# Performance work log

Hardware: AMD Instinct MI355X
Metric: run time of the kernel (lower is better)

The kernel has to match this reference:

```python
import jax, jax.numpy as jnp
import numpy as np

N = 50000      # nodes
E = 800000     # edges (avg degree 16)
IN_DIM = 128
HID = 64       # num_hidden
HEADS = 1
NUM_LAYERS = 3       # -> 4 SNATConv layers total
SLOPE = 0.2          # negative_slope
THR = 0.01           # threhold: edges with attention < THR are pruned after layer 0


def setup_inputs() -> dict:
    key = jax.random.key(0)
    ks = jax.random.split(key, 16)
    s = 0.05
    x = jax.random.normal(ks[0], (N, IN_DIM), jnp.float32)
    edge_src = jax.random.randint(ks[1], (E,), 0, N)
    edge_dst = jax.random.randint(ks[2], (E,), 0, N)
    W_embed = jax.random.normal(ks[3], (IN_DIM, HID), jnp.float32) * s
    n_conv = NUM_LAYERS + 1
    # all conv layers map HID*HEADS -> HEADS*HID (heads==1 so square)
    W_gat = jax.random.normal(ks[4], (n_conv, HID, HEADS * HID), jnp.float32) * s
    a_l = jax.random.normal(ks[5], (n_conv, HEADS, HID), jnp.float32) * s
    a_r = jax.random.normal(ks[6], (n_conv, HEADS, HID), jnp.float32) * s
    d_cat = (NUM_LAYERS + 1) * HID
    W0 = jax.random.normal(ks[7], (d_cat, HID), jnp.float32) * s
    b0 = jnp.zeros((HID,), jnp.float32)
    W1 = jax.random.normal(ks[8], (HID, HID), jnp.float32) * s
    b1 = jnp.zeros((HID,), jnp.float32)
    W2 = jax.random.normal(ks[9], (HID, 1), jnp.float32) * s
    b2 = jnp.zeros((1,), jnp.float32)
    return {"x": x, "edge_src": edge_src, "edge_dst": edge_dst,
            "W_embed": W_embed, "W_gat": W_gat, "a_l": a_l, "a_r": a_r,
            "W0": W0, "b0": b0, "W1": W1, "b1": b1, "W2": W2, "b2": b2}


def _edge_softmax(e, dst):
    # e: [E, H] raw scores; softmax over incoming edges of each dst node
    m = jax.ops.segment_max(e, dst, num_segments=N)       # [N, H]
    a = jnp.exp(e - m[dst])
    s = jax.ops.segment_sum(a, dst, num_segments=N)       # [N, H]
    return a / jnp.maximum(s[dst], 1e-9)


def _snat_conv(h, W, al, ar, src, dst, mask):
    # h: [N, F_in]; W: [F_in, H*HID]; al/ar: [H, HID]
    feat = (h @ W).reshape(N, HEADS, HID)                 # [N, H, HID]
    el = jnp.sum(feat * al, axis=-1)                      # [N, H]
    er = jnp.sum(feat * ar, axis=-1)
    e = jax.nn.leaky_relu(el[src] + er[dst], SLOPE)       # [E, H]
    if mask is not None:
        e = jnp.where(mask, e, -1e9)                      # prune thresholded edges
    alpha = _edge_softmax(e, dst)                         # [E, H]
    out = jax.ops.segment_sum(feat[src] * alpha[..., None], dst, num_segments=N)
    return jax.nn.elu(out), alpha                         # [N, H, HID], [E, H]


def reference(x, edge_src, edge_dst, W_embed, W_gat, a_l, a_r, W0, b0, W1, b1, W2, b2):
    src, dst = edge_src, edge_dst
    h = jnp.tanh(x @ W_embed)                             # [N, HID]
    # layer 0: computes attention and the threshold mask (index_1 / index_0)
    h0, alpha = _snat_conv(h, W_gat[0], a_l[0], a_r[0], src, dst, None)
    mask = alpha >= THR                                   # [E, H] kept-edge mask
    h = h0.reshape(N, HEADS * HID)
    H_cat = [h]
    for l in range(1, NUM_LAYERS):                        # middle layers reuse mask
        hl, _ = _snat_conv(h, W_gat[l], a_l[l], a_r[l], src, dst, mask)
        h = hl.reshape(N, HEADS * HID)
        H_cat.append(h)
    feats, _ = _snat_conv(h, W_gat[NUM_LAYERS], a_l[NUM_LAYERS], a_r[NUM_LAYERS], src, dst, mask)
    feats = feats.mean(axis=1)                            # [N, HID] mean over heads
    f = jnp.concatenate(H_cat + [feats], axis=1)          # [N, (L+1)*HID]
    out = jax.nn.relu(f @ W0 + b0)                        # activationP
    out = jax.nn.relu(out @ W1 + b1)
    out = jax.nn.relu(out @ W2 + b2)                      # final F.relu
    return out                                            # [N, 1]
```

## Files before the change

kernel.cpp:

```cpp
#include <hip/hip_runtime.h>
#include <math.h>


__global__ void k_zero(int* __restrict__ counts, int N) {
  int i = blockIdx.x * 256 + threadIdx.x;
  if (i < N) counts[i] = 0;
}

__global__ void k_hist(const int* __restrict__ dst, int* __restrict__ counts, int E) {
  int e = blockIdx.x * blockDim.x + threadIdx.x;
  if (e < E) atomicAdd(&counts[dst[e]], 1);
}

__global__ __launch_bounds__(1024) void k_bsum(const int* __restrict__ counts,
                                               int* __restrict__ bsum, int n) {
  __shared__ int wsum[16];
  int tid = threadIdx.x, lane = tid & 63, wid = tid >> 6;
  int i = blockIdx.x * 1024 + tid;
  int v = (i < n) ? counts[i] : 0;
  #pragma unroll
  for (int off = 32; off; off >>= 1) v += __shfl_xor(v, off, 64);
  if (lane == 0) wsum[wid] = v;
  __syncthreads();
  if (wid == 0) {
    int w = (lane < 16) ? wsum[lane] : 0;
    #pragma unroll
    for (int off = 8; off; off >>= 1) w += __shfl_xor(w, off, 64);
    if (lane == 0) bsum[blockIdx.x] = w;
  }
}

__global__ __launch_bounds__(64) void k_bscan(const int* __restrict__ bsum,
                                              int* __restrict__ bofs,
                                              int* __restrict__ row_ptr,
                                              int nb, int n) {
  int lane = threadIdx.x;
  int carry = 0;
  for (int base = 0; base < nb; base += 64) {
    int idx = base + lane;
    int orig = (idx < nb) ? bsum[idx] : 0;
    int inc = orig;
    #pragma unroll
    for (int off = 1; off < 64; off <<= 1) {
      int t = __shfl_up(inc, off, 64);
      if (lane >= off) inc += t;
    }
    if (idx < nb) bofs[idx] = carry + inc - orig;
    carry += __shfl(inc, 63, 64);
  }
  if (lane == 0) row_ptr[n] = carry;
}

__global__ __launch_bounds__(1024) void k_scan3(const int* __restrict__ counts,
                                                const int* __restrict__ bofs,
                                                int* __restrict__ row_ptr,
                                                int* __restrict__ cursor, int n) {
  __shared__ int wsum[16];
  int tid = threadIdx.x, lane = tid & 63, wid = tid >> 6;
  int i = blockIdx.x * 1024 + tid;
  int v = (i < n) ? counts[i] : 0;
  int inc = v;
  #pragma unroll
  for (int off = 1; off < 64; off <<= 1) {
    int t = __shfl_up(inc, off, 64);
    if (lane >= off) inc += t;
  }
  if (lane == 63) wsum[wid] = inc;
  __syncthreads();
  if (wid == 0 && lane < 16) {
    int orig = wsum[lane];
    int w = orig;
    #pragma unroll
    for (int off = 1; off < 16; off <<= 1) {
      int t = __shfl_up(w, off, 64);
      if (lane >= off) w += t;
    }
    wsum[lane] = w - orig;
  }
  __syncthreads();
  int excl = bofs[blockIdx.x] + wsum[wid] + inc - v;
  if (i < n) { row_ptr[i] = excl; cursor[i] = excl; }
}

__global__ void k_scatter(const int* __restrict__ src, const int* __restrict__ dst,
                          int* __restrict__ cursor, int* __restrict__ csr_src, int E) {
  int e = blockIdx.x * blockDim.x + threadIdx.x;
  if (e < E) {
    int pos = atomicAdd(&cursor[dst[e]], 1);
    csr_src[pos] = src[e];
  }
}

#define SWS 68

#define STAGE_W(DST, SRC)                                            \
  {                                                                  \
    int k_ = threadIdx.x >> 2, p_ = threadIdx.x & 3;                 \
    const float* s_ = (SRC) + k_ * 64 + p_ * 16;                     \
    float* d_ = (DST) + k_ * SWS + p_ * 16;                          \
    _Pragma("unroll")                                                \
    for (int c_ = 0; c_ < 4; c_++)                                   \
      *(float4*)(d_ + c_ * 4) = *(const float4*)(s_ + c_ * 4);       \
  }

#define GEMM64(ACC, ABASE, ASTRIDE, KOFF)                            \
  { _Pragma("unroll 4")                                              \
    for (int k_ = 0; k_ < 64; k_++) {                                \
      float4 w4_ = *(const float4*)&sW[k_ * SWS + fq];               \
      float a0_ = (ABASE)[(nr +  0) * (ASTRIDE) + (KOFF) + k_];      \
      float a1_ = (ABASE)[(nr + 16) * (ASTRIDE) + (KOFF) + k_];      \
      float a2_ = (ABASE)[(nr + 32) * (ASTRIDE) + (KOFF) + k_];      \
      float a3_ = (ABASE)[(nr + 48) * (ASTRIDE) + (KOFF) + k_];      \
      ACC[0][0] = fmaf(a0_, w4_.x, ACC[0][0]);                       \
      ACC[0][1] = fmaf(a0_, w4_.y, ACC[0][1]);                       \
      ACC[0][2] = fmaf(a0_, w4_.z, ACC[0][2]);                       \
      ACC[0][3] = fmaf(a0_, w4_.w, ACC[0][3]);                       \
      ACC[1][0] = fmaf(a1_, w4_.x, ACC[1][0]);                       \
      ACC[1][1] = fmaf(a1_, w4_.y, ACC[1][1]);                       \
      ACC[1][2] = fmaf(a1_, w4_.z, ACC[1][2]);                       \
      ACC[1][3] = fmaf(a1_, w4_.w, ACC[1][3]);                       \
      ACC[2][0] = fmaf(a2_, w4_.x, ACC[2][0]);                       \
      ACC[2][1] = fmaf(a2_, w4_.y, ACC[2][1]);                       \
      ACC[2][2] = fmaf(a2_, w4_.z, ACC[2][2]);                       \
      ACC[2][3] = fmaf(a2_, w4_.w, ACC[2][3]);                       \
      ACC[3][0] = fmaf(a3_, w4_.x, ACC[3][0]);                       \
      ACC[3][1] = fmaf(a3_, w4_.y, ACC[3][1]);                       \
      ACC[3][2] = fmaf(a3_, w4_.z, ACC[3][2]);                       \
      ACC[3][3] = fmaf(a3_, w4_.w, ACC[3][3]);                       \
    } }

__global__ __launch_bounds__(256, 3) void k_embed_feat(
    const float* __restrict__ x, const float* __restrict__ We,
    const float* __restrict__ Wg, const float* __restrict__ al,
    const float* __restrict__ ar, float* __restrict__ feat,
    float* __restrict__ el, float* __restrict__ er, int N) {
  __shared__ float sA[64 * 129];
  __shared__ float sW[64 * SWS];
  __shared__ float sE[64 * 8];
  int tid = threadIdx.x, lane = tid & 63, wv = tid >> 6;
  int nb0 = blockIdx.x * 64, nl = N - 1;
  int r = tid >> 2, p = tid & 3;
  int nr = lane >> 2, fc = lane & 3;
  int fq = wv * 16 + fc * 4;
  {
    const float* gp = x + (size_t)min(nb0 + r, nl) * 128;
    #pragma unroll
    for (int half = 0; half < 2; half++) {
      const float* g = gp + half * 64 + p * 16;
      float4 v0 = *(const float4*)(g + 0), v1 = *(const float4*)(g + 4);
      float4 v2 = *(const float4*)(g + 8), v3 = *(const float4*)(g + 12);
      float* dp = &sA[r * 129 + half * 64 + p * 16];
      dp[0]=v0.x; dp[1]=v0.y; dp[2]=v0.z; dp[3]=v0.w;
      dp[4]=v1.x; dp[5]=v1.y; dp[6]=v1.z; dp[7]=v1.w;
      dp[8]=v2.x; dp[9]=v2.y; dp[10]=v2.z; dp[11]=v2.w;
      dp[12]=v3.x; dp[13]=v3.y; dp[14]=v3.z; dp[15]=v3.w;
    }
  }
  STAGE_W(sW, We);
  __syncthreads();
  float acc[4][4];
  #pragma unroll
  for (int m = 0; m < 4; m++)
    #pragma unroll
    for (int j = 0; j < 4; j++) acc[m][j] = 0.f;
  GEMM64(acc, sA, 129, 0);
  __syncthreads();
  STAGE_W(sW, We + 4096);
  __syncthreads();
  GEMM64(acc, sA, 129, 64);
  __syncthreads();
  STAGE_W(sW, Wg);
  #pragma unroll
  for (int m = 0; m < 4; m++)
    #pragma unroll
    for (int j = 0; j < 4; j++)
      sA[(nr + 16 * m) * 65 + fq + j] = tanhf(acc[m][j]);
  __syncthreads();
  float acc2[4][4];
  #pragma unroll
  for (int m = 0; m < 4; m++)
    #pragma unroll
    for (int j = 0; j < 4; j++) acc2[m][j] = 0.f;
  GEMM64(acc2, sA, 65, 0);
  {
    float alv[4], arv[4];
    *(float4*)&alv[0] = *(const float4*)(al + fq);
    *(float4*)&arv[0] = *(const float4*)(ar + fq);
    #pragma unroll
    for (int m = 0; m < 4; m++) {
      float pl = 0.f, pr = 0.f;
      #pragma unroll
      for (int j = 0; j < 4; j++) {
        pl = fmaf(acc2[m][j], alv[j], pl);
        pr = fmaf(acc2[m][j], arv[j], pr);
      }
      pl += __shfl_xor(pl, 1, 64); pl += __shfl_xor(pl, 2, 64);
      pr += __shfl_xor(pr, 1, 64); pr += __shfl_xor(pr, 2, 64);
      if (fc == 0) {
        sE[(nr + 16 * m) * 8 + wv] = pl;
        sE[(nr + 16 * m) * 8 + 4 + wv] = pr;
      }
    }
  }
  __syncthreads();
  #pragma unroll
  for (int m = 0; m < 4; m++)
    #pragma unroll
    for (int j = 0; j < 4; j++)
      sA[(nr + 16 * m) * 65 + fq + j] = acc2[m][j];
  __syncthreads();
  {
    int n = nb0 + r;
    if (n < N) {
      const float* sp = &sA[r * 65 + p * 16];
      float* gp = feat + (size_t)n * 64 + p * 16;
      #pragma unroll
      for (int q = 0; q < 4; q++)
        *(float4*)(gp + q * 4) = make_float4(sp[q*4+0], sp[q*4+1], sp[q*4+2], sp[q*4+3]);
    }
  }
  if (tid < 64) {
    int n = nb0 + tid;
    if (n < N) {
      el[n] = (sE[tid*8+0] + sE[tid*8+1]) + (sE[tid*8+2] + sE[tid*8+3]);
      er[n] = (sE[tid*8+4] + sE[tid*8+5]) + (sE[tid*8+6] + sE[tid*8+7]);
    }
  }
}

__global__ __launch_bounds__(256, 3) void k_feat(const float* __restrict__ hin,
                                                 const float* __restrict__ Wg,
                                                 const float* __restrict__ al,
                                                 const float* __restrict__ ar,
                                                 float* __restrict__ feat,
                                                 float* __restrict__ el,
                                                 float* __restrict__ er, int N) {
  __shared__ float sA[64 * 65];
  __shared__ float sW[64 * SWS];
  __shared__ float sE[64 * 8];
  int tid = threadIdx.x, lane = tid & 63, wv = tid >> 6;
  int nb0 = blockIdx.x * 64;
  int nl = N - 1;
  int r = tid >> 2, p = tid & 3;
  int nr = lane >> 2, fc = lane & 3;
  int fq = wv * 16 + fc * 4;
  {
    const float* g = hin + (size_t)min(nb0 + r, nl) * 64 + p * 16;
    float4 v0 = *(const float4*)(g + 0), v1 = *(const float4*)(g + 4);
    float4 v2 = *(const float4*)(g + 8), v3 = *(const float4*)(g + 12);
    float* dp = &sA[r * 65 + p * 16];
    dp[0]=v0.x; dp[1]=v0.y; dp[2]=v0.z; dp[3]=v0.w;
    dp[4]=v1.x; dp[5]=v1.y; dp[6]=v1.z; dp[7]=v1.w;
    dp[8]=v2.x; dp[9]=v2.y; dp[10]=v2.z; dp[11]=v2.w;
    dp[12]=v3.x; dp[13]=v3.y; dp[14]=v3.z; dp[15]=v3.w;
  }
  STAGE_W(sW, Wg);
  __syncthreads();
  float acc[4][4];
  #pragma unroll
  for (int m = 0; m < 4; m++)
    #pragma unroll
    for (int j = 0; j < 4; j++) acc[m][j] = 0.f;
  GEMM64(acc, sA, 65, 0);
  {
    float alv[4], arv[4];
    *(float4*)&alv[0] = *(const float4*)(al + fq);
    *(float4*)&arv[0] = *(const float4*)(ar + fq);
    #pragma unroll
    for (int m = 0; m < 4; m++) {
      float pl = 0.f, pr = 0.f;
      #pragma unroll
      for (int j = 0; j < 4; j++) {
        pl = fmaf(acc[m][j], alv[j], pl);
        pr = fmaf(acc[m][j], arv[j], pr);
      }
      pl += __shfl_xor(pl, 1, 64); pl += __shfl_xor(pl, 2, 64);
      pr += __shfl_xor(pr, 1, 64); pr += __shfl_xor(pr, 2, 64);
      if (fc == 0) {
        sE[(nr + 16 * m) * 8 + wv] = pl;
        sE[(nr + 16 * m) * 8 + 4 + wv] = pr;
      }
    }
  }
  __syncthreads();
  #pragma unroll
  for (int m = 0; m < 4; m++)
    #pragma unroll
    for (int j = 0; j < 4; j++)
      sA[(nr + 16 * m) * 65 + fq + j] = acc[m][j];
  __syncthreads();
  {
    int n = nb0 + r;
    if (n < N) {
      const float* sp = &sA[r * 65 + p * 16];
      float* gp = feat + (size_t)n * 64 + p * 16;
      #pragma unroll
      for (int q = 0; q < 4; q++)
        *(float4*)(gp + q * 4) = make_float4(sp[q*4+0], sp[q*4+1], sp[q*4+2], sp[q*4+3]);
    }
  }
  if (tid < 64) {
    int n = nb0 + tid;
    if (n < N) {
      el[n] = (sE[tid*8+0] + sE[tid*8+1]) + (sE[tid*8+2] + sE[tid*8+3]);
      er[n] = (sE[tid*8+4] + sE[tid*8+5]) + (sE[tid*8+6] + sE[tid*8+7]);
    }
  }
}

__global__ __launch_bounds__(256) void k_aggr(const float* __restrict__ feat,
                                              const float* __restrict__ el,
                                              const float* __restrict__ er,
                                              const int* __restrict__ row_ptr,
                                              const int* __restrict__ csr_src,
                                              unsigned char* __restrict__ mask,
                                              int write_mask, int use_mask,
                                              float* __restrict__ hout, int N) {
  __shared__ __align__(16) int   su[4][64];
  __shared__ __align__(16) float spl[4][64];
  int wv = (int)((blockIdx.x * blockDim.x + threadIdx.x) >> 6);
  int wave = threadIdx.x >> 6, lane = threadIdx.x & 63;
  if (wv >= N) return;
  int beg = row_ptr[wv], end = row_ptr[wv + 1];
  int deg = end - beg;
  float erv = er[wv];
  float acc0 = 0.f, acc1 = 0.f, acc2 = 0.f, acc3 = 0.f;
  if (deg <= 64) {
    int k = beg + lane;
    bool have = (lane < deg);
    int u = have ? csr_src[k] : 0;
    float sc = -INFINITY;
    if (have) {
      float e0 = el[u] + erv;
      sc = (e0 >= 0.f) ? e0 : 0.2f * e0;
      if (use_mask && mask[k] == 0) sc = -1e9f;
    }
    float m = sc;
    #pragma unroll
    for (int off = 32; off; off >>= 1) m = fmaxf(m, __shfl_xor(m, off, 64));
    float pl = have ? expf(sc - m) : 0.f;
    float s = pl;
    #pragma unroll
    for (int off = 32; off; off >>= 1) s += __shfl_xor(s, off, 64);
    pl *= 1.0f / fmaxf(s, 1e-9f);
    if (write_mask && have) mask[k] = (pl >= 0.01f) ? 1 : 0;
    su[wave][lane] = u;
    spl[wave][lane] = pl;
    int dq = (deg + 3) >> 2;
    #pragma unroll 2
    for (int q = 0; q < dq; q++) {
      int4   uu = *(const int4*)&su[wave][q * 4];
      float4 pp = *(const float4*)&spl[wave][q * 4];
      acc0 = fmaf(pp.x, feat[(size_t)uu.x * 64 + lane], acc0);
      acc1 = fmaf(pp.y, feat[(size_t)uu.y * 64 + lane], acc1);
      acc2 = fmaf(pp.z, feat[(size_t)uu.z * 64 + lane], acc2);
      acc3 = fmaf(pp.w, feat[(size_t)uu.w * 64 + lane], acc3);
    }
  } else {
    float m = -INFINITY, s = 0.f;
    for (int base = beg; base < end; base += 64) {
      int k = base + lane;
      float sc = -INFINITY;
      if (k < end) {
        int u = csr_src[k];
        float e0 = el[u] + erv;
        sc = (e0 >= 0.f) ? e0 : 0.2f * e0;
        if (use_mask && mask[k] == 0) sc = -1e9f;
      }
      float cm = sc;
      #pragma unroll
      for (int off = 32; off; off >>= 1) cm = fmaxf(cm, __shfl_xor(cm, off, 64));
      float nm = fmaxf(m, cm);
      float t = (k < end) ? expf(sc - nm) : 0.f;
      #pragma unroll
      for (int off = 32; off; off >>= 1) t += __shfl_xor(t, off, 64);
      s = s * expf(m - nm) + t;
      m = nm;
    }
    float inv = 1.0f / fmaxf(s, 1e-9f);
    for (int base = beg; base < end; base += 64) {
      int k = base + lane;
      int u = 0;
      float pl = 0.f;
      if (k < end) {
        u = csr_src[k];
        float e0 = el[u] + erv;
        float sc = (e0 >= 0.f) ? e0 : 0.2f * e0;
        if (use_mask && mask[k] == 0) sc = -1e9f;
        pl = expf(sc - m) * inv;
        if (write_mask) mask[k] = (pl >= 0.01f) ? 1 : 0;
      }
      su[wave][lane] = u;
      spl[wave][lane] = pl;
      int cnt = min(64, end - base);
      int dq = (cnt + 3) >> 2;
      for (int q = 0; q < dq; q++) {
        int4   uu = *(const int4*)&su[wave][q * 4];
        float4 pp = *(const float4*)&spl[wave][q * 4];
        acc0 = fmaf(pp.x, feat[(size_t)uu.x * 64 + lane], acc0);
        acc1 = fmaf(pp.y, feat[(size_t)uu.y * 64 + lane], acc1);
        acc2 = fmaf(pp.z, feat[(size_t)uu.z * 64 + lane], acc2);
        acc3 = fmaf(pp.w, feat[(size_t)uu.w * 64 + lane], acc3);
      }
    }
  }
  float acc = (acc0 + acc1) + (acc2 + acc3);
  hout[(size_t)wv * 64 + lane] = (acc > 0.f) ? acc : expm1f(acc);
}

__global__ __launch_bounds__(256, 3) void k_mlp(const float* __restrict__ o0,
                                                const float* __restrict__ o1,
                                                const float* __restrict__ o2,
                                                const float* __restrict__ o3,
                                                const float* __restrict__ W0,
                                                const float* __restrict__ b0,
                                                const float* __restrict__ W1,
                                                const float* __restrict__ b1,
                                                const float* __restrict__ W2,
                                                const float* __restrict__ b2,
                                                float* __restrict__ out, int N) {
  __shared__ float sA[64 * 65];
  __shared__ float sW[64 * SWS];
  __shared__ float sR[64 * 5];
  int tid = threadIdx.x, lane = tid & 63, wv = tid >> 6;
  int nb0 = blockIdx.x * 64;
  int nl = N - 1;
  int r = tid >> 2, p = tid & 3;
  int nr = lane >> 2, fc = lane & 3;
  int fq = wv * 16 + fc * 4;
  float acc[4][4];
  {
    float4 b0v = *(const float4*)(b0 + fq);
    #pragma unroll
    for (int m = 0; m < 4; m++) {
      acc[m][0] = b0v.x; acc[m][1] = b0v.y;
      acc[m][2] = b0v.z; acc[m][3] = b0v.w;
    }
  }

  auto seg = [&](const float* __restrict__ sp, const float* __restrict__ wp) {
    __syncthreads();
    {
      const float* g = sp + (size_t)min(nb0 + r, nl) * 64 + p * 16;
      float4 v0 = *(const float4*)(g + 0), v1 = *(const float4*)(g + 4);
      float4 v2 = *(const float4*)(g + 8), v3 = *(const float4*)(g + 12);
      float* dp = &sA[r * 65 + p * 16];
      dp[0]=v0.x; dp[1]=v0.y; dp[2]=v0.z; dp[3]=v0.w;
      dp[4]=v1.x; dp[5]=v1.y; dp[6]=v1.z; dp[7]=v1.w;
      dp[8]=v2.x; dp[9]=v2.y; dp[10]=v2.z; dp[11]=v2.w;
      dp[12]=v3.x; dp[13]=v3.y; dp[14]=v3.z; dp[15]=v3.w;
    }
    STAGE_W(sW, wp);
    __syncthreads();
    GEMM64(acc, sA, 65, 0);
  };
  seg(o0, W0);
  seg(o1, W0 + 64 * 64);
  seg(o2, W0 + 128 * 64);
  seg(o3, W0 + 192 * 64);

  __syncthreads();
  STAGE_W(sW, W1);
  #pragma unroll
  for (int m = 0; m < 4; m++)
    #pragma unroll
    for (int j = 0; j < 4; j++) {
      float z = acc[m][j];
      sA[(nr + 16 * m) * 65 + fq + j] = (z > 0.f) ? z : 0.f;
    }
  __syncthreads();
  float a1[4][4];
  {
    float4 b1v = *(const float4*)(b1 + fq);
    #pragma unroll
    for (int m = 0; m < 4; m++) {
      a1[m][0] = b1v.x; a1[m][1] = b1v.y;
      a1[m][2] = b1v.z; a1[m][3] = b1v.w;
    }
  }
  GEMM64(a1, sA, 65, 0);
  {
    float4 w2v = *(const float4*)(W2 + fq);
    float w2a[4] = {w2v.x, w2v.y, w2v.z, w2v.w};
    #pragma unroll
    for (int m = 0; m < 4; m++) {
      float rp = 0.f;
      #pragma unroll
      for (int j = 0; j < 4; j++) {
        float t = (a1[m][j] > 0.f) ? a1[m][j] : 0.f;
        rp = fmaf(t, w2a[j], rp);
      }
      rp += __shfl_xor(rp, 1, 64); rp += __shfl_xor(rp, 2, 64);
      if (fc == 0) sR[(nr + 16 * m) * 5 + wv] = rp;
    }
  }
  __syncthreads();
  if (tid < 64) {
    int n = nb0 + tid;
    if (n < N) {
      float o = (sR[tid*5+0] + sR[tid*5+1]) + (sR[tid*5+2] + sR[tid*5+3]) + b2[0];
      out[n] = (o > 0.f) ? o : 0.f;
    }
  }
}

extern "C" void kernel_launch(void* const* d_in, const int* in_sizes, int n_in,
                              void* d_out, int out_size, void* d_ws, size_t ws_size,
                              hipStream_t stream) {
  const float* x       = (const float*)d_in[0];
  const int*   esrc    = (const int*)d_in[1];
  const int*   edst    = (const int*)d_in[2];
  const float* W_embed = (const float*)d_in[3];
  const float* W_gat   = (const float*)d_in[4];
  const float* a_l     = (const float*)d_in[5];
  const float* a_r     = (const float*)d_in[6];
  const float* W0      = (const float*)d_in[7];
  const float* b0      = (const float*)d_in[8];
  const float* W1      = (const float*)d_in[9];
  const float* b1      = (const float*)d_in[10];
  const float* W2      = (const float*)d_in[11];
  const float* b2      = (const float*)d_in[12];
  float* out = (float*)d_out;
  const int N = in_sizes[0] / 128;
  const int E = in_sizes[1];

  char* p = (char*)d_ws;
  auto alloc = [&](size_t bytes) -> char* {
    char* r = p;
    p += (bytes + 255) & ~(size_t)255;
    return r;
  };
  float* out0 = (float*)alloc((size_t)N * 64 * 4);
  float* out1 = (float*)alloc((size_t)N * 64 * 4);
  float* out2 = (float*)alloc((size_t)N * 64 * 4);
  float* out3 = (float*)alloc((size_t)N * 64 * 4);
  float* feat = (float*)alloc((size_t)N * 64 * 4);
  float* el   = (float*)alloc((size_t)N * 4);
  float* er   = (float*)alloc((size_t)N * 4);
  int* counts  = (int*)alloc((size_t)N * 4);
  int* row_ptr = (int*)alloc((size_t)(N + 1) * 4);
  int* cursor  = (int*)alloc((size_t)N * 4);
  int* csr_src = (int*)alloc((size_t)E * 4);
  unsigned char* mask = (unsigned char*)alloc((size_t)E);
  int nb = (N + 1023) / 1024;
  int* bsum = (int*)alloc((size_t)nb * 4);
  int* bofs = (int*)alloc((size_t)nb * 4);

  k_zero<<<(N + 255) / 256, 256, 0, stream>>>(counts, N);
  k_hist<<<(E + 255) / 256, 256, 0, stream>>>(edst, counts, E);
  k_bsum<<<nb, 1024, 0, stream>>>(counts, bsum, N);
  k_bscan<<<1, 64, 0, stream>>>(bsum, bofs, row_ptr, nb, N);
  k_scan3<<<nb, 1024, 0, stream>>>(counts, bofs, row_ptr, cursor, N);
  k_scatter<<<(E + 255) / 256, 256, 0, stream>>>(esrc, edst, cursor, csr_src, E);

  int dgb = (N + 63) / 64;

  k_embed_feat<<<dgb, 256, 0, stream>>>(x, W_embed, W_gat,
                                        a_l, a_r, feat, el, er, N);
  float* outs[4] = {out0, out1, out2, out3};
  k_aggr<<<(N + 3) / 4, 256, 0, stream>>>(feat, el, er, row_ptr, csr_src, mask,
                                          1, 0, out0, N);

  for (int l = 1; l < 4; l++) {
    k_feat<<<dgb, 256, 0, stream>>>(outs[l - 1], W_gat + (size_t)l * 4096,
                                    a_l + (size_t)l * 64, a_r + (size_t)l * 64,
                                    feat, el, er, N);
    k_aggr<<<(N + 3) / 4, 256, 0, stream>>>(feat, el, er, row_ptr, csr_src, mask,
                                            0, 1, outs[l], N);
  }

  k_mlp<<<dgb, 256, 0, stream>>>(out0, out1, out2, out3, W0, b0,
                                 W1, b1, W2, b2, out, N);
}
```

Baseline: 452.6 us.

## Build CSR via bucketed two-pass binning with LDS atomics instead of global scatter

The single global-atomic scatter into CSR is replaced by a two-level counting sort. Edges are first counted and binned into buckets of 128 destination nodes, each split into 8 sub-bins keyed by block group to spread atomic contention. Per-bucket blocks then place edges into their final CSR slots using shared-memory cursors. This aims to cut the cost of random global atomics and scattered writes, at the price of extra kernels, an intermediate int2 buffer, an extra atomic per edge in the histogram, and a serial single-wave scan.

```diff
diff --git a/kernel.cpp b/kernel.cpp
--- a/kernel.cpp
+++ b/kernel.cpp
@@ -2,14 +2,21 @@
 #include <math.h>
 
 
-__global__ void k_zero(int* __restrict__ counts, int N) {
+__global__ void k_zero(int* __restrict__ counts, int* __restrict__ cntA,
+                       int N, int nbg) {
   int i = blockIdx.x * 256 + threadIdx.x;
   if (i < N) counts[i] = 0;
-}
-
-__global__ void k_hist(const int* __restrict__ dst, int* __restrict__ counts, int E) {
+  if (i < nbg) cntA[i] = 0;
+}
+
+__global__ void k_hist2(const int* __restrict__ dst, int* __restrict__ counts,
+                        int* __restrict__ cntA, int E) {
   int e = blockIdx.x * blockDim.x + threadIdx.x;
-  if (e < E) atomicAdd(&counts[dst[e]], 1);
+  if (e < E) {
+    int d = dst[e];
+    atomicAdd(&counts[d], 1);
+    atomicAdd(&cntA[(d >> 7) * 8 + ((e >> 10) & 7)], 1);
+  }
 }
 
 __global__ __launch_bounds__(1024) void k_bsum(const int* __restrict__ counts,
@@ -53,8 +60,7 @@
 
 __global__ __launch_bounds__(1024) void k_scan3(const int* __restrict__ counts,
                                                 const int* __restrict__ bofs,
-                                                int* __restrict__ row_ptr,
-                                                int* __restrict__ cursor, int n) {
+                                                int* __restrict__ row_ptr, int n) {
   __shared__ int wsum[16];
   int tid = threadIdx.x, lane = tid & 63, wid = tid >> 6;
   int i = blockIdx.x * 1024 + tid;
@@ -79,15 +85,78 @@
   }
   __syncthreads();
   int excl = bofs[blockIdx.x] + wsum[wid] + inc - v;
-  if (i < n) { row_ptr[i] = excl; cursor[i] = excl; }
-}
-
-__global__ void k_scatter(const int* __restrict__ src, const int* __restrict__ dst,
-                          int* __restrict__ cursor, int* __restrict__ csr_src, int E) {
-  int e = blockIdx.x * blockDim.x + threadIdx.x;
-  if (e < E) {
-    int pos = atomicAdd(&cursor[dst[e]], 1);
-    csr_src[pos] = src[e];
+  if (i < n) row_ptr[i] = excl;
+}
+
+__global__ __launch_bounds__(64) void k_scanA(const int* __restrict__ cntA,
+                                              int* __restrict__ ofsA,
+                                              int* __restrict__ curA,
+                                              int nbg, int E) {
+  int lane = threadIdx.x;
+  int carry = 0;
+  for (int base = 0; base < nbg; base += 64) {
+    int idx = base + lane;
+    int orig = (idx < nbg) ? cntA[idx] : 0;
+    int inc = orig;
+    #pragma unroll
+    for (int off = 1; off < 64; off <<= 1) {
+      int t = __shfl_up(inc, off, 64);
+      if (lane >= off) inc += t;
+    }
+    if (idx < nbg) {
+      int ex = carry + inc - orig;
+      ofsA[idx] = ex;
+      curA[idx] = ex;
+    }
+    carry += __shfl(inc, 63, 64);
+  }
+  if (lane == 0) ofsA[nbg] = E;
+}
+
+__global__ __launch_bounds__(256) void k_bin(const int* __restrict__ src,
+                                             const int* __restrict__ dst,
+                                             int* __restrict__ curA,
+                                             int2* __restrict__ tmp, int E) {
+  int g = blockIdx.x & 7;
+  int e0 = blockIdx.x * 1024 + threadIdx.x * 4;
+  if (e0 >= E) return;
+  if (e0 + 3 < E) {
+    int4 s4 = *(const int4*)(src + e0);
+    int4 d4 = *(const int4*)(dst + e0);
+    int s[4] = {s4.x, s4.y, s4.z, s4.w};
+    int d[4] = {d4.x, d4.y, d4.z, d4.w};
+    #pragma unroll
+    for (int i = 0; i < 4; i++) {
+      int pos = atomicAdd(&curA[(d[i] >> 7) * 8 + g], 1);
+      tmp[pos] = make_int2(s[i], d[i]);
+    }
+  } else {
+    for (int i = 0; i < 4 && e0 + i < E; i++) {
+      int sv = src[e0 + i], dv = dst[e0 + i];
+      int pos = atomicAdd(&curA[(dv >> 7) * 8 + g], 1);
+      tmp[pos] = make_int2(sv, dv);
+    }
+  }
+}
+
+__global__ __launch_bounds__(256) void k_csr(const int2* __restrict__ tmp,
+                                             const int* __restrict__ ofsA,
+                                             const int* __restrict__ row_ptr,
+                                             int* __restrict__ csr_src,
+                                             int N, int nbuk) {
+  __shared__ int lcur[128];
+  int b = blockIdx.x;
+  int lo = b << 7;
+  int hi = min(lo + 128, N);
+  int tid = threadIdx.x;
+  if (tid < hi - lo) lcur[tid] = row_ptr[lo + tid];
+  __syncthreads();
+  int beg = ofsA[b * 8];
+  int end = ofsA[(b + 1) * 8];
+  for (int i = beg + tid; i < end; i += 256) {
+    int2 e = tmp[i];
+    int pos = atomicAdd(&lcur[e.y - lo], 1);
+    csr_src[pos] = e.x;
   }
 }
 
@@ -539,19 +608,26 @@
   float* er   = (float*)alloc((size_t)N * 4);
   int* counts  = (int*)alloc((size_t)N * 4);
   int* row_ptr = (int*)alloc((size_t)(N + 1) * 4);
-  int* cursor  = (int*)alloc((size_t)N * 4);
   int* csr_src = (int*)alloc((size_t)E * 4);
   unsigned char* mask = (unsigned char*)alloc((size_t)E);
   int nb = (N + 1023) / 1024;
   int* bsum = (int*)alloc((size_t)nb * 4);
   int* bofs = (int*)alloc((size_t)nb * 4);
-
-  k_zero<<<(N + 255) / 256, 256, 0, stream>>>(counts, N);
-  k_hist<<<(E + 255) / 256, 256, 0, stream>>>(edst, counts, E);
+  int nbuk = (N + 127) >> 7;
+  int nbg = nbuk * 8;
+  int* cntA = (int*)alloc((size_t)nbg * 4);
+  int* ofsA = (int*)alloc((size_t)(nbg + 1) * 4);
+  int* curA = (int*)alloc((size_t)nbg * 4);
+  int2* tmp = (int2*)alloc((size_t)E * 8);
+
+  k_zero<<<(N + 255) / 256, 256, 0, stream>>>(counts, cntA, N, nbg);
+  k_hist2<<<(E + 255) / 256, 256, 0, stream>>>(edst, counts, cntA, E);
   k_bsum<<<nb, 1024, 0, stream>>>(counts, bsum, N);
   k_bscan<<<1, 64, 0, stream>>>(bsum, bofs, row_ptr, nb, N);
-  k_scan3<<<nb, 1024, 0, stream>>>(counts, bofs, row_ptr, cursor, N);
-  k_scatter<<<(E + 255) / 256, 256, 0, stream>>>(esrc, edst, cursor, csr_src, E);
+  k_scan3<<<nb, 1024, 0, stream>>>(counts, bofs, row_ptr, N);
+  k_scanA<<<1, 64, 0, stream>>>(cntA, ofsA, curA, nbg, E);
+  k_bin<<<(E + 1023) / 1024, 256, 0, stream>>>(esrc, edst, curA, tmp, E);
+  k_csr<<<nbuk, 256, 0, stream>>>(tmp, ofsA, row_ptr, csr_src, N, nbuk);
 
   int dgb = (N + 63) / 64;
 
```

Measured after the change: 588.4 us. 30.0% more time.

## Build CSR with partitioned LDS-atomic histogram and scatter kernels

Applied to the files above, without the earlier changes.

Replaces the global-atomic histogram and scatter with 32 blocks that each own a range of destination nodes and keep counts and cursors in shared memory. Every block streams the full edge list and only processes edges that land in its range. This removes global atomics and the zero and cursor buffers, but each block reads all E edges, only 32 blocks run on a large GPU, and the shared array is hard-coded to 1600 entries, which ties it to N of 50000.

```diff
diff --git a/kernel.cpp b/kernel.cpp
--- a/kernel.cpp
+++ b/kernel.cpp
@@ -2,15 +2,7 @@
 #include <math.h>
 
 
-__global__ void k_zero(int* __restrict__ counts, int N) {
-  int i = blockIdx.x * 256 + threadIdx.x;
-  if (i < N) counts[i] = 0;
-}
-
-__global__ void k_hist(const int* __restrict__ dst, int* __restrict__ counts, int E) {
-  int e = blockIdx.x * blockDim.x + threadIdx.x;
-  if (e < E) atomicAdd(&counts[dst[e]], 1);
-}
+#define NPART 32
 
 __global__ __launch_bounds__(1024) void k_bsum(const int* __restrict__ counts,
                                                int* __restrict__ bsum, int n) {
@@ -53,8 +45,7 @@
 
 __global__ __launch_bounds__(1024) void k_scan3(const int* __restrict__ counts,
                                                 const int* __restrict__ bofs,
-                                                int* __restrict__ row_ptr,
-                                                int* __restrict__ cursor, int n) {
+                                                int* __restrict__ row_ptr, int n) {
   __shared__ int wsum[16];
   int tid = threadIdx.x, lane = tid & 63, wid = tid >> 6;
   int i = blockIdx.x * 1024 + tid;
@@ -79,15 +70,64 @@
   }
   __syncthreads();
   int excl = bofs[blockIdx.x] + wsum[wid] + inc - v;
-  if (i < n) { row_ptr[i] = excl; cursor[i] = excl; }
-}
-
-__global__ void k_scatter(const int* __restrict__ src, const int* __restrict__ dst,
-                          int* __restrict__ cursor, int* __restrict__ csr_src, int E) {
-  int e = blockIdx.x * blockDim.x + threadIdx.x;
-  if (e < E) {
-    int pos = atomicAdd(&cursor[dst[e]], 1);
-    csr_src[pos] = src[e];
+  if (i < n) row_ptr[i] = excl;
+}
+
+__global__ __launch_bounds__(256) void k_pcount(const int* __restrict__ dst,
+                                                int* __restrict__ counts,
+                                                int N, int E) {
+  __shared__ int lcnt[1600];
+  int b = blockIdx.x;
+  int per = (N + NPART - 1) / NPART;
+  int lo = b * per, hi = min(lo + per, N);
+  int len = hi - lo;
+  int tid = threadIdx.x;
+  for (int i = tid; i < len; i += 256) lcnt[i] = 0;
+  __syncthreads();
+  int e4 = E >> 2;
+  const int4* d4 = (const int4*)dst;
+  for (int i = tid; i < e4; i += 256) {
+    int4 d = d4[i];
+    if (d.x >= lo && d.x < hi) atomicAdd(&lcnt[d.x - lo], 1);
+    if (d.y >= lo && d.y < hi) atomicAdd(&lcnt[d.y - lo], 1);
+    if (d.z >= lo && d.z < hi) atomicAdd(&lcnt[d.z - lo], 1);
+    if (d.w >= lo && d.w < hi) atomicAdd(&lcnt[d.w - lo], 1);
+  }
+  for (int e = (e4 << 2) + tid; e < E; e += 256) {
+    int d = dst[e];
+    if (d >= lo && d < hi) atomicAdd(&lcnt[d - lo], 1);
+  }
+  __syncthreads();
+  for (int i = tid; i < len; i += 256) counts[lo + i] = lcnt[i];
+}
+
+__global__ __launch_bounds__(256) void k_pscatter(const int* __restrict__ src,
+                                                  const int* __restrict__ dst,
+                                                  const int* __restrict__ row_ptr,
+                                                  int* __restrict__ csr_src,
+                                                  int N, int E) {
+  __shared__ int lcur[1600];
+  int b = blockIdx.x;
+  int per = (N + NPART - 1) / NPART;
+  int lo = b * per, hi = min(lo + per, N);
+  int len = hi - lo;
+  int tid = threadIdx.x;
+  for (int i = tid; i < len; i += 256) lcur[i] = row_ptr[lo + i];
+  __syncthreads();
+  int e4 = E >> 2;
+  const int4* d4 = (const int4*)dst;
+  const int4* s4 = (const int4*)src;
+  for (int i = tid; i < e4; i += 256) {
+    int4 d = d4[i];
+    int4 s = s4[i];
+    if (d.x >= lo && d.x < hi) csr_src[atomicAdd(&lcur[d.x - lo], 1)] = s.x;
+    if (d.y >= lo && d.y < hi) csr_src[atomicAdd(&lcur[d.y - lo], 1)] = s.y;
+    if (d.z >= lo && d.z < hi) csr_src[atomicAdd(&lcur[d.z - lo], 1)] = s.z;
+    if (d.w >= lo && d.w < hi) csr_src[atomicAdd(&lcur[d.w - lo], 1)] = s.w;
+  }
+  for (int e = (e4 << 2) + tid; e < E; e += 256) {
+    int d = dst[e];
+    if (d >= lo && d < hi) csr_src[atomicAdd(&lcur[d - lo], 1)] = src[e];
   }
 }
 
@@ -539,19 +579,17 @@
   float* er   = (float*)alloc((size_t)N * 4);
   int* counts  = (int*)alloc((size_t)N * 4);
   int* row_ptr = (int*)alloc((size_t)(N + 1) * 4);
-  int* cursor  = (int*)alloc((size_t)N * 4);
   int* csr_src = (int*)alloc((size_t)E * 4);
   unsigned char* mask = (unsigned char*)alloc((size_t)E);
   int nb = (N + 1023) / 1024;
   int* bsum = (int*)alloc((size_t)nb * 4);
   int* bofs = (int*)alloc((size_t)nb * 4);
 
-  k_zero<<<(N + 255) / 256, 256, 0, stream>>>(counts, N);
-  k_hist<<<(E + 255) / 256, 256, 0, stream>>>(edst, counts, E);
+  k_pcount<<<NPART, 256, 0, stream>>>(edst, counts, N, E);
   k_bsum<<<nb, 1024, 0, stream>>>(counts, bsum, N);
   k_bscan<<<1, 64, 0, stream>>>(bsum, bofs, row_ptr, nb, N);
-  k_scan3<<<nb, 1024, 0, stream>>>(counts, bofs, row_ptr, cursor, N);
-  k_scatter<<<(E + 255) / 256, 256, 0, stream>>>(esrc, edst, cursor, csr_src, E);
+  k_scan3<<<nb, 1024, 0, stream>>>(counts, bofs, row_ptr, N);
+  k_pscatter<<<NPART, 256, 0, stream>>>(esrc, edst, row_ptr, csr_src, N, E);
 
   int dgb = (N + 63) / 64;
 
```

New measurement: 1.134 ms. 2.51x slower.
